# Kernel optimization log

Measured on AMD Instinct MI355X. Metric: run time of the kernel, lower is better.

## Reference

```python
import jax, jax.numpy as jnp
import numpy as np

B, S, H, F, E, TOPK = 4, 2048, 1024, 4096, 8, 2

def setup_inputs() -> dict:
    key = jax.random.key(0)
    ks = jax.random.split(key, 8)
    sh = 1.0 / np.sqrt(H)
    sf = 1.0 / np.sqrt(F)
    return {
        "hidden_states": jax.random.normal(ks[0], (B, S, H), jnp.float32),
        "Wr": jax.random.normal(ks[1], (H, E), jnp.float32) * sh,
        "br": jnp.zeros((E,), jnp.float32),
        "W1": jax.random.normal(ks[2], (E, H, F), jnp.float32) * sh,
        "b1": jax.random.normal(ks[3], (E, F), jnp.float32) * 0.01,
        "W2": jax.random.normal(ks[4], (E, F, H), jnp.float32) * sf,
        "b2": jax.random.normal(ks[5], (E, H), jnp.float32) * 0.01,
    }

def reference(hidden_states, Wr, br, W1, b1, W2, b2):
    b, s, h = hidden_states.shape
    x = hidden_states.reshape(-1, h)                      # [T, H]
    T = x.shape[0]
    logits = x @ Wr + br                                  # [T, E]
    routing_weights = jax.nn.softmax(logits, axis=-1)     # [T, E]
    top_v, top_i = jax.lax.top_k(logits, TOPK)            # [T, k]
    top_gates = jax.nn.softmax(top_v, axis=-1)            # [T, k]
    rows = jnp.arange(T)[:, None]
    dispatch = jnp.zeros((T, E), logits.dtype).at[rows, top_i].set(top_gates)  # [T, E]
    # Each expert runs densely on gate-scaled tokens: gelu((g*x)@W1 + b1)@W2 + b2.
    # (g*x)@W1 == g * (x@W1), so share the first GEMM across experts.
    z = jnp.einsum('th,ehf->etf', x, W1)                  # [E, T, F]
    a = jax.nn.gelu(dispatch.T[:, :, None] * z + b1[:, None, :], approximate=False)
    expert_out = jnp.einsum('etf,efh->eth', a, W2) + b2[:, None, :]  # [E, T, H]
    combined = jnp.einsum('te,eth->th', dispatch, expert_out)        # [T, H]
    final_output = combined.reshape(b, s, h)
    aux_loss = jnp.sum(routing_weights.mean(axis=0) * (dispatch.sum(axis=0) / T)) * E
    return (final_output,
            routing_weights.reshape(b, s, E),
            dispatch.reshape(b, s, E),
            aux_loss,
            logits.reshape(b, s, E))
```

## Files before the change

kernel.cpp:

```cpp
#include <hip/hip_runtime.h>

#define T_TOK 8192
#define H_DIM 1024
#define F_DIM 4096
#define E_NUM 8

typedef __attribute__((ext_vector_type(8))) short short8;
typedef __attribute__((ext_vector_type(4))) float f32x4;

__device__ __forceinline__ unsigned short f2bf(float f) {
  unsigned int u = __float_as_uint(f);
  return (unsigned short)((u + 0x7fffu + ((u >> 16) & 1u)) >> 16);
}

__device__ __forceinline__ float bf2f(unsigned short u) {
  return __uint_as_float((unsigned int)u << 16);
}

__device__ __forceinline__ float gelu_f(float v) {
  float z = 0.7978845608028654f * fmaf(0.044715f * v * v, v, v);
  z = fminf(fmaxf(z, -12.0f), 12.0f);
  const float ez = __expf(-2.0f * z);
  const float t = (1.0f - ez) / (1.0f + ez);
  return 0.5f * v * (1.0f + t);
}

__device__ __forceinline__ void gload16(const void* g, void* l) {
  __builtin_amdgcn_global_load_lds(
      (__attribute__((address_space(1))) const unsigned int*)(unsigned long long)g,
      (__attribute__((address_space(3))) unsigned int*)(unsigned int)(unsigned long long)l,
      16, 0, 0);
}

__global__ __launch_bounds__(256) void k_transpose_cvt(const float* __restrict__ in,
                                                       unsigned short* __restrict__ out,
                                                       int R, int C) {
  __shared__ float tile[64][33];
  const size_t eoff = (size_t)blockIdx.z * R * C;
  const int c0 = blockIdx.x * 32, r0 = blockIdx.y * 64;
  const int tx = threadIdx.x & 31, ty = threadIdx.x >> 5;
#pragma unroll
  for (int i = 0; i < 8; ++i)
    tile[ty + i * 8][tx] = in[eoff + (size_t)(r0 + ty + i * 8) * C + (c0 + tx)];
  __syncthreads();
  const int ow = threadIdx.x & 63, oc = threadIdx.x >> 6;
#pragma unroll
  for (int i = 0; i < 8; ++i)
    out[eoff + (size_t)(c0 + oc + i * 4) * R + (r0 + ow)] = f2bf(tile[ow][oc + i * 4]);
}

__global__ __launch_bounds__(256) void k_logits(const float* __restrict__ x,
                                                const float* __restrict__ Wr,
                                                const float* __restrict__ br,
                                                double* __restrict__ ld,
                                                float* __restrict__ out_logits,
                                                unsigned short* __restrict__ xb) {
  const int lane = threadIdx.x & 63;
  const int t = blockIdx.x * 4 + (threadIdx.x >> 6);
  double acc[8] = {0, 0, 0, 0, 0, 0, 0, 0};
#pragma unroll
  for (int i = 0; i < 16; ++i) {
    const int h = i * 64 + lane;
    const float xv = x[(size_t)t * H_DIM + h];
    xb[(size_t)t * H_DIM + h] = f2bf(xv);
    const float4 wa = ((const float4*)Wr)[h * 2];
    const float4 wb = ((const float4*)Wr)[h * 2 + 1];
    acc[0] += (double)xv * wa.x; acc[1] += (double)xv * wa.y;
    acc[2] += (double)xv * wa.z; acc[3] += (double)xv * wa.w;
    acc[4] += (double)xv * wb.x; acc[5] += (double)xv * wb.y;
    acc[6] += (double)xv * wb.z; acc[7] += (double)xv * wb.w;
  }
#pragma unroll
  for (int e = 0; e < 8; ++e)
#pragma unroll
    for (int m = 32; m; m >>= 1) acc[e] += __shfl_xor(acc[e], m);
  if (lane == 0) {
#pragma unroll
    for (int e = 0; e < 8; ++e) {
      const double l = acc[e] + (double)br[e];
      ld[(size_t)t * 8 + e] = l;
      out_logits[(size_t)t * 8 + e] = (float)l;
    }
  }
}

__global__ __launch_bounds__(256) void k_decide(const double* __restrict__ ld,
                                                float* __restrict__ out_rw,
                                                float* __restrict__ out_disp,
                                                int* __restrict__ cnt,
                                                int* __restrict__ bidx,
                                                float* __restrict__ bgate,
                                                float* __restrict__ sums,
                                                int* __restrict__ slotmap) {
  __shared__ int hcnt[8];
  __shared__ int hbase[8];
  __shared__ float srw[8];
  __shared__ float sds[8];
  const int tloc = threadIdx.x;
  const int t = blockIdx.x * 256 + tloc;
  const int lane = tloc & 63;
  if (tloc < 8) { hcnt[tloc] = 0; srw[tloc] = 0.0f; sds[tloc] = 0.0f; }
  __syncthreads();

  double l[8];
#pragma unroll
  for (int e = 0; e < 8; ++e) l[e] = ld[(size_t)t * 8 + e];
  double mx = l[0];
#pragma unroll
  for (int e = 1; e < 8; ++e) mx = l[e] > mx ? l[e] : mx;
  double ex[8], se = 0.0;
#pragma unroll
  for (int e = 0; e < 8; ++e) { ex[e] = exp(l[e] - mx); se += ex[e]; }
  int i1 = 0;
#pragma unroll
  for (int e = 1; e < 8; ++e) if (l[e] > l[i1]) i1 = e;
  int i2 = (i1 == 0) ? 1 : 0;
#pragma unroll
  for (int e = 0; e < 8; ++e) if (e != i1 && l[e] > l[i2]) i2 = e;
  const double g1 = 1.0 / (1.0 + exp(l[i2] - l[i1]));
  const double g2 = 1.0 - g1;

  float rwv[8];
#pragma unroll
  for (int e = 0; e < 8; ++e) {
    rwv[e] = (float)(ex[e] / se);
    out_rw[(size_t)t * 8 + e] = rwv[e];
    out_disp[(size_t)t * 8 + e] = (e == i1) ? (float)g1 : (e == i2) ? (float)g2 : 0.0f;
  }
#pragma unroll
  for (int e = 0; e < 8; ++e) {
    float v = rwv[e];
#pragma unroll
    for (int m = 32; m; m >>= 1) v += __shfl_xor(v, m);
    if (lane == 0) atomicAdd(&srw[e], v);
  }
  atomicAdd(&sds[i1], (float)g1);
  atomicAdd(&sds[i2], (float)g2);

  const int loc1 = atomicAdd(&hcnt[i1], 1);
  const int loc2 = atomicAdd(&hcnt[i2], 1);
  __syncthreads();
  if (tloc < 8) hbase[tloc] = atomicAdd(&cnt[tloc], hcnt[tloc]);
  __syncthreads();
  const int s1 = hbase[i1] + loc1;
  const int s2 = hbase[i2] + loc2;
  bidx[i1 * T_TOK + s1] = t; bgate[i1 * T_TOK + s1] = (float)g1;
  bidx[i2 * T_TOK + s2] = t; bgate[i2 * T_TOK + s2] = (float)g2;
  slotmap[t * 2]     = (i1 << 16) | s1;
  slotmap[t * 2 + 1] = (i2 << 16) | s2;
  if (tloc < 8) {
    atomicAdd(&sums[tloc], srw[tloc]);
    atomicAdd(&sums[8 + tloc], sds[tloc]);
  }
}

__global__ void k_prefix_aux(const int* __restrict__ cnt, int* __restrict__ abase,
                             const float* __restrict__ sums, float* __restrict__ out_aux) {
  if (threadIdx.x == 0) {
    int base = 0;
    for (int e = 0; e < 8; ++e) { abase[e] = base; base += (cnt[e] + 127) & ~127; }
    abase[8] = base;
    double aux = 0.0;
    for (int e = 0; e < 8; ++e) aux += ((double)sums[e] / 8192.0) * ((double)sums[8 + e] / 8192.0);
    *out_aux = (float)(aux * 8.0);
  }
}

#define MFMA_Q(qm_, qn_, Bset_)                                                        \
  do {                                                                                 \
    _Pragma("unroll") for (int kh = 0; kh < 2; ++kh)                                   \
    _Pragma("unroll") for (int mi = 0; mi < 4; ++mi)                                   \
    _Pragma("unroll") for (int ni = 0; ni < 2; ++ni)                                   \
      acc[(qm_)*4 + mi][(qn_)*2 + ni] = __builtin_amdgcn_mfma_f32_16x16x32_bf16(       \
          Areg[mi][kh], Bset_[ni][kh], acc[(qm_)*4 + mi][(qn_)*2 + ni], 0, 0, 0);      \
  } while (0)

#define LOAD_A(mh_)                                                                    \
  do {                                                                                 \
    const char* Ab = smem + slot * 65536 + (mh_)*16384;                                \
    _Pragma("unroll") for (int mi = 0; mi < 4; ++mi) {                                 \
      Areg[mi][0] = *(const short8*)(Ab + mi * 2048 + aoffk0);                         \
      Areg[mi][1] = *(const short8*)(Ab + mi * 2048 + aoffk1);                         \
    }                                                                                  \
  } while (0)

#define LOAD_B(set_, nh_)                                                              \
  do {                                                                                 \
    const char* Bb = smem + slot * 65536 + 32768 + (nh_)*16384;                        \
    _Pragma("unroll") for (int ni = 0; ni < 2; ++ni) {                                 \
      set_[ni][0] = *(const short8*)(Bb + ni * 2048 + boffk0);                         \
      set_[ni][1] = *(const short8*)(Bb + ni * 2048 + boffk1);                         \
    }                                                                                  \
  } while (0)

#define PHASE_TAIL(MFMA_STMT)                                                          \
  __builtin_amdgcn_s_barrier();                                                        \
  __builtin_amdgcn_s_setprio(1);                                                       \
  MFMA_STMT;                                                                           \
  __builtin_amdgcn_s_setprio(0);                                                       \
  __builtin_amdgcn_s_barrier();

__global__ __launch_bounds__(512, 2) void k_gemm1(
    const unsigned short* __restrict__ xb, const unsigned short* __restrict__ w1t,
    const float* __restrict__ b1, const int* __restrict__ bidx,
    const float* __restrict__ bgate, const int* __restrict__ abase,
    unsigned short* __restrict__ abuf) {
  constexpr int NT = 16;
  const int e = blockIdx.z, by = blockIdx.y, bx = blockIdx.x;
  const int pb = abase[e], pcnt = abase[e + 1] - pb;
  if (by * 256 >= pcnt) return;
  __shared__ char smem[131072];
  const int tid = threadIdx.x, wid = tid >> 6, lane = tid & 63;
  const int wr = wid >> 2, wc = wid & 3;
  const int rr0 = tid >> 3;
  const int kbyte = ((tid & 7) ^ (rr0 & 7)) * 16;
  const int d0 = tid * 16, d1 = d0 + 8192;

  const int* bidx_e = bidx + e * T_TOK + by * 256;
  int tok[4];
#pragma unroll
  for (int i = 0; i < 4; ++i) tok[i] = bidx_e[i * 64 + rr0];

  const int brB0 = ((rr0 >> 5) * 64 + (rr0 & 31));
  const char* Bbase = (const char*)(w1t + (size_t)e * F_DIM * H_DIM + (size_t)(bx * 256) * H_DIM);

#define G1_STAGE_A(g_, mh_)                                                            \
  do {                                                                                 \
    const char* s0 = (const char*)(xb + (size_t)tok[(mh_)] * H_DIM) + (g_)*128 + kbyte;\
    const char* s1 = (const char*)(xb + (size_t)tok[2 + (mh_)] * H_DIM) + (g_)*128 + kbyte; \
    char* dst = smem + (((g_)&1) * 65536) + (mh_)*16384;                               \
    gload16(s0, dst + d0); gload16(s1, dst + d1);                                      \
  } while (0)

#define G1_STAGE_B(g_, nh_)                                                            \
  do {                                                                                 \
    const char* s0 = Bbase + (size_t)(brB0 + (nh_)*32) * 2048 + (g_)*128 + kbyte;      \
    const char* s1 = Bbase + (size_t)(brB0 + 128 + (nh_)*32) * 2048 + (g_)*128 + kbyte;\
    char* dst = smem + (((g_)&1) * 65536) + 32768 + (nh_)*16384;                       \
    gload16(s0, dst + d0); gload16(s1, dst + d1);                                      \
  } while (0)

  const int aoffk0 = (wr * 64 + (lane & 15)) * 128 + (((lane >> 4) ^ (lane & 7)) * 16);
  const int aoffk1 = aoffk0 ^ 64;
  const int boffk0 = (wc * 32 + (lane & 15)) * 128 + (((lane >> 4) ^ (lane & 7)) * 16);
  const int boffk1 = boffk0 ^ 64;

  f32x4 acc[8][4] = {};
  short8 Areg[4][2], B0reg[2][2], B1reg[2][2];

  G1_STAGE_A(0, 0); G1_STAGE_B(0, 1); G1_STAGE_A(0, 1); G1_STAGE_B(0, 0);
  G1_STAGE_A(1, 0); G1_STAGE_B(1, 1); G1_STAGE_A(1, 1);
  asm volatile("s_waitcnt vmcnt(6)" ::: "memory");
  __builtin_amdgcn_sched_barrier(0);
  __builtin_amdgcn_s_barrier();

  for (int g = 0; g < NT; ++g) {
    const int slot = g & 1;
    LOAD_A(0); LOAD_B(B0reg, 0);
    if (g + 1 < NT) G1_STAGE_B(g + 1, 0);
    PHASE_TAIL(MFMA_Q(0, 0, B0reg));
    LOAD_B(B1reg, 1);
    if (g + 2 < NT) G1_STAGE_A(g + 2, 0);
    PHASE_TAIL(MFMA_Q(0, 1, B1reg));
    LOAD_A(1);
    if (g + 2 < NT) G1_STAGE_B(g + 2, 1);
    PHASE_TAIL(MFMA_Q(1, 1, B1reg));
    if (g + 2 < NT) {
      G1_STAGE_A(g + 2, 1);
      asm volatile("s_waitcnt vmcnt(6)" ::: "memory");
    } else if (g + 1 < NT) {
      asm volatile("s_waitcnt vmcnt(0)" ::: "memory");
    }
    __builtin_amdgcn_sched_barrier(0);
    PHASE_TAIL(MFMA_Q(1, 0, B0reg));
  }

  const int lcol = lane & 15;
  const int gcol0 = bx * 256 + wc * 64;
  float b1v[4];
#pragma unroll
  for (int n = 0; n < 4; ++n) b1v[n] = b1[(size_t)e * F_DIM + gcol0 + n * 16 + lcol];
  const float* bg_e = bgate + e * T_TOK + by * 256;
#pragma unroll
  for (int m = 0; m < 8; ++m) {
    const int rl = wr * 128 + m * 16 + (lane >> 4) * 4;
#pragma unroll
    for (int j = 0; j < 4; ++j) {
      const int row = rl + j;
      if (by * 256 + row < pcnt) {
        const float gt = bg_e[row];
        unsigned short* orow = abuf + (size_t)(pb + by * 256 + row) * F_DIM + gcol0;
#pragma unroll
        for (int n = 0; n < 4; ++n) {
          const float v = fmaf(gt, acc[m][n][j], b1v[n]);
          orow[n * 16 + lcol] = f2bf(gelu_f(v));
        }
      }
    }
  }
#undef G1_STAGE_A
#undef G1_STAGE_B
}

__global__ __launch_bounds__(512, 2) void k_gemm2(
    const unsigned short* __restrict__ abuf, const unsigned short* __restrict__ w2t,
    const float* __restrict__ b2, const float* __restrict__ bgate,
    const int* __restrict__ abase, unsigned short* __restrict__ eout_a,
    unsigned short* __restrict__ eout_b, int split) {
  const int ez = blockIdx.z;
  const int e = ez & 7, ks = ez >> 3;
  const int by = blockIdx.y, bx = blockIdx.x;
  const int pb = abase[e], pcnt = abase[e + 1] - pb;
  if (by * 256 >= pcnt) return;
  const int g0 = ks * 32;
  const int gend = split ? (g0 + 32) : 64;
  unsigned short* eo = ks ? eout_b : eout_a;
  __shared__ char smem[131072];
  const int tid = threadIdx.x, wid = tid >> 6, lane = tid & 63;
  const int wr = wid >> 2, wc = wid & 3;
  const int rr0 = tid >> 3;
  const int kbyte = ((tid & 7) ^ (rr0 & 7)) * 16;
  const int d0 = tid * 16, d1 = d0 + 8192;
  const int aoffk0 = (wr * 64 + (lane & 15)) * 128 + (((lane >> 4) ^ (lane & 7)) * 16);
  const int aoffk1 = aoffk0 ^ 64;
  const int boffk0 = (wc * 32 + (lane & 15)) * 128 + (((lane >> 4) ^ (lane & 7)) * 16);
  const int boffk1 = boffk0 ^ 64;

  const char* Abase = (const char*)(abuf + (size_t)(pb + by * 256) * F_DIM);
  const int brB0 = ((rr0 >> 5) * 64 + (rr0 & 31));
  const char* Bbase = (const char*)(w2t + (size_t)e * H_DIM * F_DIM + (size_t)(bx * 256) * F_DIM);

#define G2_STAGE_A(g_, mh_)                                                            \
  do {                                                                                 \
    const char* s0 = Abase + (size_t)((mh_)*64 + rr0) * 8192 + (g_)*128 + kbyte;       \
    const char* s1 = Abase + (size_t)(128 + (mh_)*64 + rr0) * 8192 + (g_)*128 + kbyte; \
    char* dst = smem + (((g_)&1) * 65536) + (mh_)*16384;                               \
    gload16(s0, dst + d0); gload16(s1, dst + d1);                                      \
  } while (0)

#define G2_STAGE_B(g_, nh_)                                                            \
  do {                                                                                 \
    const char* s0 = Bbase + (size_t)(brB0 + (nh_)*32) * 8192 + (g_)*128 + kbyte;      \
    const char* s1 = Bbase + (size_t)(brB0 + 128 + (nh_)*32) * 8192 + (g_)*128 + kbyte;\
    char* dst = smem + (((g_)&1) * 65536) + 32768 + (nh_)*16384;                       \
    gload16(s0, dst + d0); gload16(s1, dst + d1);                                      \
  } while (0)

  f32x4 acc[8][4] = {};
  short8 Areg[4][2], B0reg[2][2], B1reg[2][2];

  G2_STAGE_A(g0, 0); G2_STAGE_B(g0, 1); G2_STAGE_A(g0, 1); G2_STAGE_B(g0, 0);
  G2_STAGE_A(g0 + 1, 0); G2_STAGE_B(g0 + 1, 1); G2_STAGE_A(g0 + 1, 1);
  asm volatile("s_waitcnt vmcnt(6)" ::: "memory");
  __builtin_amdgcn_sched_barrier(0);
  __builtin_amdgcn_s_barrier();

  for (int g = g0; g < gend; ++g) {
    const int slot = g & 1;
    LOAD_A(0); LOAD_B(B0reg, 0);
    if (g + 1 < gend) G2_STAGE_B(g + 1, 0);
    PHASE_TAIL(MFMA_Q(0, 0, B0reg));
    LOAD_B(B1reg, 1);
    if (g + 2 < gend) G2_STAGE_A(g + 2, 0);
    PHASE_TAIL(MFMA_Q(0, 1, B1reg));
    LOAD_A(1);
    if (g + 2 < gend) G2_STAGE_B(g + 2, 1);
    PHASE_TAIL(MFMA_Q(1, 1, B1reg));
    if (g + 2 < gend) {
      G2_STAGE_A(g + 2, 1);
      asm volatile("s_waitcnt vmcnt(6)" ::: "memory");
    } else if (g + 1 < gend) {
      asm volatile("s_waitcnt vmcnt(0)" ::: "memory");
    }
    __builtin_amdgcn_sched_barrier(0);
    PHASE_TAIL(MFMA_Q(1, 0, B0reg));
  }

  const int lcol = lane & 15;
  const int gcol0 = bx * 256 + wc * 64;
  float b2v[4];
#pragma unroll
  for (int n = 0; n < 4; ++n)
    b2v[n] = (ks == 0) ? b2[(size_t)e * H_DIM + gcol0 + n * 16 + lcol] : 0.0f;
  const float* bg_e = bgate + e * T_TOK;
#pragma unroll
  for (int m = 0; m < 8; ++m) {
    const int rl = wr * 128 + m * 16 + (lane >> 4) * 4;
#pragma unroll
    for (int j = 0; j < 4; ++j) {
      const int gm = by * 256 + rl + j;
      if (gm < pcnt) {
        const float gt = bg_e[gm];
        unsigned short* orow = eo + (size_t)(pb + gm) * H_DIM + gcol0;
#pragma unroll
        for (int n = 0; n < 4; ++n)
          orow[n * 16 + lcol] = f2bf((acc[m][n][j] + b2v[n]) * gt);
      }
    }
  }
#undef G2_STAGE_A
#undef G2_STAGE_B
}

__global__ __launch_bounds__(256) void k_combine(const unsigned short* __restrict__ ea,
                                                 const unsigned short* __restrict__ eb,
                                                 const int* __restrict__ slotmap,
                                                 const int* __restrict__ abase,
                                                 float* __restrict__ outf, int split) {
  const int t = blockIdx.x;
  const int c = threadIdx.x;
  const int v0 = slotmap[t * 2], v1 = slotmap[t * 2 + 1];
  const size_t row0 = (size_t)(abase[v0 >> 16] + (v0 & 0xffff)) * H_DIM;
  const size_t row1 = (size_t)(abase[v1 >> 16] + (v1 & 0xffff)) * H_DIM;
  uint2 a = ((const uint2*)(ea + row0))[c];
  uint2 b = ((const uint2*)(ea + row1))[c];
  float r0 = bf2f(a.x & 0xffff) + bf2f(b.x & 0xffff);
  float r1 = bf2f(a.x >> 16)    + bf2f(b.x >> 16);
  float r2 = bf2f(a.y & 0xffff) + bf2f(b.y & 0xffff);
  float r3 = bf2f(a.y >> 16)    + bf2f(b.y >> 16);
  if (split) {
    uint2 p = ((const uint2*)(eb + row0))[c];
    uint2 q = ((const uint2*)(eb + row1))[c];
    r0 += bf2f(p.x & 0xffff) + bf2f(q.x & 0xffff);
    r1 += bf2f(p.x >> 16)    + bf2f(q.x >> 16);
    r2 += bf2f(p.y & 0xffff) + bf2f(q.y & 0xffff);
    r3 += bf2f(p.y >> 16)    + bf2f(q.y >> 16);
  }
  ((float4*)outf)[(size_t)t * 256 + c] = make_float4(r0, r1, r2, r3);
}

extern "C" void kernel_launch(void* const* d_in, const int* in_sizes, int n_in,
                              void* d_out, int out_size, void* d_ws, size_t ws_size,
                              hipStream_t stream) {
  const float* x  = (const float*)d_in[0];
  const float* Wr = (const float*)d_in[1];
  const float* br = (const float*)d_in[2];
  const float* W1 = (const float*)d_in[3];
  const float* b1 = (const float*)d_in[4];
  const float* W2 = (const float*)d_in[5];
  const float* b2 = (const float*)d_in[6];
  float* out = (float*)d_out;
  float* out_final  = out;
  float* out_rw     = out + 8388608;
  float* out_disp   = out_rw + 65536;
  float* out_aux    = out_disp + 65536;
  float* out_logits = out_aux + 1;

  char* ws = (char*)d_ws;
  unsigned short* xb   = (unsigned short*)(ws);
  unsigned short* w1t  = (unsigned short*)(ws + 16777216);
  unsigned short* w2t  = (unsigned short*)(ws + 83886080);
  unsigned short* abuf = (unsigned short*)(ws + 150994944);
  int*    bidx  = (int*)(ws + 293601280);
  float*  bgate = (float*)(ws + 293863424);
  int*    cnt   = (int*)(ws + 294125568);
  int*    abase = (int*)(ws + 294125632);
  float*  sums  = (float*)(ws + 294125696);
  double* ld    = (double*)(ws + 294125824);
  int*    slotmap = (int*)(ws + 294650112);
  unsigned short* eout_a = (unsigned short*)(ws);
  unsigned short* eout_b = (unsigned short*)(ws + 35651584);

  const int split = 1;

  hipMemsetAsync(cnt, 0, 64, stream);
  hipMemsetAsync(sums, 0, 64, stream);
  hipMemsetAsync(bidx, 0, 262144, stream);
  hipMemsetAsync(bgate, 0, 262144, stream);

  k_transpose_cvt<<<dim3(128, 16, 8), 256, 0, stream>>>(W1, w1t, H_DIM, F_DIM);
  k_transpose_cvt<<<dim3(32, 64, 8), 256, 0, stream>>>(W2, w2t, F_DIM, H_DIM);
  k_logits<<<2048, 256, 0, stream>>>(x, Wr, br, ld, out_logits, xb);
  k_decide<<<32, 256, 0, stream>>>(ld, out_rw, out_disp, cnt, bidx, bgate, sums, slotmap);
  k_prefix_aux<<<1, 64, 0, stream>>>(cnt, abase, sums, out_aux);
  k_gemm1<<<dim3(16, 12, 8), 512, 0, stream>>>(xb, w1t, b1, bidx, bgate, abase, abuf);
  k_gemm2<<<dim3(4, 32, 16), 512, 0, stream>>>(abuf, w2t, b2, bgate, abase, eout_a, eout_b, split);
  k_combine<<<8192, 256, 0, stream>>>(eout_a, eout_b, slotmap, abase, out_final, split);
}
```

Baseline: 533.1 us.

## Halve gemm1 K-tile to 32 and raise occupancy to four blocks per CU

Rewrites the gemm1 kernel to stage K-slices of 32 instead of 64, halving shared memory per block from 128KB to 64KB. Launch bounds move from 2 to 4 blocks per CU. The swizzle, load offsets and waitcnt thresholds are adjusted to match, and the loop now runs 32 iterations. The goal is more resident waves to hide global-load latency, at the cost of twice as many barriers per K and fewer registers per thread, which could cause spills with the 128-float accumulator.

```diff
diff --git a/kernel.cpp b/kernel.cpp
--- a/kernel.cpp
+++ b/kernel.cpp
@@ -166,6 +166,136 @@
   }
 }
 
+__global__ __launch_bounds__(512, 4) void k_gemm1(
+    const unsigned short* __restrict__ xb, const unsigned short* __restrict__ w1t,
+    const float* __restrict__ b1, const int* __restrict__ bidx,
+    const float* __restrict__ bgate, const int* __restrict__ abase,
+    unsigned short* __restrict__ abuf) {
+  constexpr int NT = 32;
+  const int e = blockIdx.z, by = blockIdx.y, bx = blockIdx.x;
+  const int pb = abase[e], pcnt = abase[e + 1] - pb;
+  if (by * 256 >= pcnt) return;
+  __shared__ char smem[65536];
+  const int tid = threadIdx.x, wid = tid >> 6, lane = tid & 63;
+  const int wr = wid >> 2, wc = wid & 3;
+  const int srow = tid >> 2;
+  const int kbyte = (((tid & 3) ^ ((tid >> 3) & 3))) * 16;
+  const int dst0 = tid * 16;
+
+  const int* bidx_e = bidx + e * T_TOK + by * 256;
+  const int tgrp = (tid < 256) ? 0 : 2;
+  const int tokA0 = bidx_e[(tgrp + 0) * 64 + (srow & 63)];
+  const int tokA1 = bidx_e[(tgrp + 1) * 64 + (srow & 63)];
+  const int nB = ((srow >> 5) * 64 + (srow & 31));
+  const char* Bbase = (const char*)(w1t + (size_t)e * F_DIM * H_DIM + (size_t)(bx * 256) * H_DIM);
+
+#define G1_STAGE_A(g_, mh_)                                                            \
+  do {                                                                                 \
+    const int tk = (mh_) ? tokA1 : tokA0;                                              \
+    const char* s0 = (const char*)(xb + (size_t)tk * H_DIM) + (g_)*64 + kbyte;         \
+    gload16(s0, smem + (((g_)&1) * 32768) + (mh_)*8192 + dst0);                        \
+  } while (0)
+
+#define G1_STAGE_B(g_, nh_)                                                            \
+  do {                                                                                 \
+    const char* s0 = Bbase + (size_t)(nB + (nh_)*32) * 2048 + (g_)*64 + kbyte;         \
+    gload16(s0, smem + (((g_)&1) * 32768) + 16384 + (nh_)*8192 + dst0);                \
+  } while (0)
+
+  const int kx = ((lane >> 4) ^ ((lane >> 1) & 3)) * 16;
+  const int aoff = (wr * 64 + (lane & 15)) * 64 + kx;
+  const int boff = (wc * 32 + (lane & 15)) * 64 + kx;
+
+#define G1_LOAD_A(mh_)                                                                 \
+  do {                                                                                 \
+    const char* Ab = smem + slot * 32768 + (mh_)*8192;                                 \
+    _Pragma("unroll") for (int mi = 0; mi < 4; ++mi)                                   \
+      Areg[mi] = *(const short8*)(Ab + aoff + mi * 1024);                              \
+  } while (0)
+
+#define G1_LOAD_B(set_, nh_)                                                           \
+  do {                                                                                 \
+    const char* Bb = smem + slot * 32768 + 16384 + (nh_)*8192;                         \
+    _Pragma("unroll") for (int ni = 0; ni < 2; ++ni)                                   \
+      set_[ni] = *(const short8*)(Bb + boff + ni * 1024);                              \
+  } while (0)
+
+#define G1_MFMA_Q(qm_, qn_, Bset_)                                                     \
+  do {                                                                                 \
+    _Pragma("unroll") for (int mi = 0; mi < 4; ++mi)                                   \
+    _Pragma("unroll") for (int ni = 0; ni < 2; ++ni)                                   \
+      acc[(qm_)*4 + mi][(qn_)*2 + ni] = __builtin_amdgcn_mfma_f32_16x16x32_bf16(       \
+          Areg[mi], Bset_[ni], acc[(qm_)*4 + mi][(qn_)*2 + ni], 0, 0, 0);              \
+  } while (0)
+
+#define G1_TAIL(MFMA_STMT)                                                             \
+  __builtin_amdgcn_s_barrier();                                                        \
+  __builtin_amdgcn_s_setprio(1);                                                       \
+  MFMA_STMT;                                                                           \
+  __builtin_amdgcn_s_setprio(0);                                                       \
+  __builtin_amdgcn_s_barrier();
+
+  f32x4 acc[8][4] = {};
+  short8 Areg[4], B0reg[2], B1reg[2];
+
+  G1_STAGE_A(0, 0); G1_STAGE_B(0, 1); G1_STAGE_A(0, 1); G1_STAGE_B(0, 0);
+  G1_STAGE_A(1, 0); G1_STAGE_B(1, 1); G1_STAGE_A(1, 1);
+  asm volatile("s_waitcnt vmcnt(3)" ::: "memory");
+  __builtin_amdgcn_sched_barrier(0);
+  __builtin_amdgcn_s_barrier();
+
+  for (int g = 0; g < NT; ++g) {
+    const int slot = g & 1;
+    G1_LOAD_A(0); G1_LOAD_B(B0reg, 0);
+    if (g + 1 < NT) G1_STAGE_B(g + 1, 0);
+    G1_TAIL(G1_MFMA_Q(0, 0, B0reg));
+    G1_LOAD_B(B1reg, 1);
+    if (g + 2 < NT) G1_STAGE_A(g + 2, 0);
+    G1_TAIL(G1_MFMA_Q(0, 1, B1reg));
+    G1_LOAD_A(1);
+    if (g + 2 < NT) G1_STAGE_B(g + 2, 1);
+    G1_TAIL(G1_MFMA_Q(1, 1, B1reg));
+    if (g + 2 < NT) {
+      G1_STAGE_A(g + 2, 1);
+      asm volatile("s_waitcnt vmcnt(3)" ::: "memory");
+    } else if (g + 1 < NT) {
+      asm volatile("s_waitcnt vmcnt(0)" ::: "memory");
+    }
+    __builtin_amdgcn_sched_barrier(0);
+    G1_TAIL(G1_MFMA_Q(1, 0, B0reg));
+  }
+
+  const int lcol = lane & 15;
+  const int gcol0 = bx * 256 + wc * 64;
+  float b1v[4];
+#pragma unroll
+  for (int n = 0; n < 4; ++n) b1v[n] = b1[(size_t)e * F_DIM + gcol0 + n * 16 + lcol];
+  const float* bg_e = bgate + e * T_TOK + by * 256;
+#pragma unroll
+  for (int m = 0; m < 8; ++m) {
+    const int rl = wr * 128 + m * 16 + (lane >> 4) * 4;
+#pragma unroll
+    for (int j = 0; j < 4; ++j) {
+      const int row = rl + j;
+      if (by * 256 + row < pcnt) {
+        const float gt = bg_e[row];
+        unsigned short* orow = abuf + (size_t)(pb + by * 256 + row) * F_DIM + gcol0;
+#pragma unroll
+        for (int n = 0; n < 4; ++n) {
+          const float v = fmaf(gt, acc[m][n][j], b1v[n]);
+          orow[n * 16 + lcol] = f2bf(gelu_f(v));
+        }
+      }
+    }
+  }
+#undef G1_STAGE_A
+#undef G1_STAGE_B
+#undef G1_LOAD_A
+#undef G1_LOAD_B
+#undef G1_MFMA_Q
+#undef G1_TAIL
+}
+
 #define MFMA_Q(qm_, qn_, Bset_)                                                        \
   do {                                                                                 \
     _Pragma("unroll") for (int kh = 0; kh < 2; ++kh)                                   \
@@ -199,108 +329,6 @@
   MFMA_STMT;                                                                           \
   __builtin_amdgcn_s_setprio(0);                                                       \
   __builtin_amdgcn_s_barrier();
-
-__global__ __launch_bounds__(512, 2) void k_gemm1(
-    const unsigned short* __restrict__ xb, const unsigned short* __restrict__ w1t,
-    const float* __restrict__ b1, const int* __restrict__ bidx,
-    const float* __restrict__ bgate, const int* __restrict__ abase,
-    unsigned short* __restrict__ abuf) {
-  constexpr int NT = 16;
-  const int e = blockIdx.z, by = blockIdx.y, bx = blockIdx.x;
-  const int pb = abase[e], pcnt = abase[e + 1] - pb;
-  if (by * 256 >= pcnt) return;
-  __shared__ char smem[131072];
-  const int tid = threadIdx.x, wid = tid >> 6, lane = tid & 63;
-  const int wr = wid >> 2, wc = wid & 3;
-  const int rr0 = tid >> 3;
-  const int kbyte = ((tid & 7) ^ (rr0 & 7)) * 16;
-  const int d0 = tid * 16, d1 = d0 + 8192;
-
-  const int* bidx_e = bidx + e * T_TOK + by * 256;
-  int tok[4];
-#pragma unroll
-  for (int i = 0; i < 4; ++i) tok[i] = bidx_e[i * 64 + rr0];
-
-  const int brB0 = ((rr0 >> 5) * 64 + (rr0 & 31));
-  const char* Bbase = (const char*)(w1t + (size_t)e * F_DIM * H_DIM + (size_t)(bx * 256) * H_DIM);
-
-#define G1_STAGE_A(g_, mh_)                                                            \
-  do {                                                                                 \
-    const char* s0 = (const char*)(xb + (size_t)tok[(mh_)] * H_DIM) + (g_)*128 + kbyte;\
-    const char* s1 = (const char*)(xb + (size_t)tok[2 + (mh_)] * H_DIM) + (g_)*128 + kbyte; \
-    char* dst = smem + (((g_)&1) * 65536) + (mh_)*16384;                               \
-    gload16(s0, dst + d0); gload16(s1, dst + d1);                                      \
-  } while (0)
-
-#define G1_STAGE_B(g_, nh_)                                                            \
-  do {                                                                                 \
-    const char* s0 = Bbase + (size_t)(brB0 + (nh_)*32) * 2048 + (g_)*128 + kbyte;      \
-    const char* s1 = Bbase + (size_t)(brB0 + 128 + (nh_)*32) * 2048 + (g_)*128 + kbyte;\
-    char* dst = smem + (((g_)&1) * 65536) + 32768 + (nh_)*16384;                       \
-    gload16(s0, dst + d0); gload16(s1, dst + d1);                                      \
-  } while (0)
-
-  const int aoffk0 = (wr * 64 + (lane & 15)) * 128 + (((lane >> 4) ^ (lane & 7)) * 16);
-  const int aoffk1 = aoffk0 ^ 64;
-  const int boffk0 = (wc * 32 + (lane & 15)) * 128 + (((lane >> 4) ^ (lane & 7)) * 16);
-  const int boffk1 = boffk0 ^ 64;
-
-  f32x4 acc[8][4] = {};
-  short8 Areg[4][2], B0reg[2][2], B1reg[2][2];
-
-  G1_STAGE_A(0, 0); G1_STAGE_B(0, 1); G1_STAGE_A(0, 1); G1_STAGE_B(0, 0);
-  G1_STAGE_A(1, 0); G1_STAGE_B(1, 1); G1_STAGE_A(1, 1);
-  asm volatile("s_waitcnt vmcnt(6)" ::: "memory");
-  __builtin_amdgcn_sched_barrier(0);
-  __builtin_amdgcn_s_barrier();
-
-  for (int g = 0; g < NT; ++g) {
-    const int slot = g & 1;
-    LOAD_A(0); LOAD_B(B0reg, 0);
-    if (g + 1 < NT) G1_STAGE_B(g + 1, 0);
-    PHASE_TAIL(MFMA_Q(0, 0, B0reg));
-    LOAD_B(B1reg, 1);
-    if (g + 2 < NT) G1_STAGE_A(g + 2, 0);
-    PHASE_TAIL(MFMA_Q(0, 1, B1reg));
-    LOAD_A(1);
-    if (g + 2 < NT) G1_STAGE_B(g + 2, 1);
-    PHASE_TAIL(MFMA_Q(1, 1, B1reg));
-    if (g + 2 < NT) {
-      G1_STAGE_A(g + 2, 1);
-      asm volatile("s_waitcnt vmcnt(6)" ::: "memory");
-    } else if (g + 1 < NT) {
-      asm volatile("s_waitcnt vmcnt(0)" ::: "memory");
-    }
-    __builtin_amdgcn_sched_barrier(0);
-    PHASE_TAIL(MFMA_Q(1, 0, B0reg));
-  }
-
-  const int lcol = lane & 15;
-  const int gcol0 = bx * 256 + wc * 64;
-  float b1v[4];
-#pragma unroll
-  for (int n = 0; n < 4; ++n) b1v[n] = b1[(size_t)e * F_DIM + gcol0 + n * 16 + lcol];
-  const float* bg_e = bgate + e * T_TOK + by * 256;
-#pragma unroll
-  for (int m = 0; m < 8; ++m) {
-    const int rl = wr * 128 + m * 16 + (lane >> 4) * 4;
-#pragma unroll
-    for (int j = 0; j < 4; ++j) {
-      const int row = rl + j;
-      if (by * 256 + row < pcnt) {
-        const float gt = bg_e[row];
-        unsigned short* orow = abuf + (size_t)(pb + by * 256 + row) * F_DIM + gcol0;
-#pragma unroll
-        for (int n = 0; n < 4; ++n) {
-          const float v = fmaf(gt, acc[m][n][j], b1v[n]);
-          orow[n * 16 + lcol] = f2bf(gelu_f(v));
-        }
-      }
-    }
-  }
-#undef G1_STAGE_A
-#undef G1_STAGE_B
-}
 
 __global__ __launch_bounds__(512, 2) void k_gemm2(
     const unsigned short* __restrict__ abuf, const unsigned short* __restrict__ w2t,
```

Result: slower. 1.736 ms (+225.7%).
